# Kernel tuning notes

Hardware: AMD Instinct MI355X
Metric: run time of the kernel (lower is better)

Reference implementation:

```python
import jax, jax.numpy as jnp
import numpy as np

BRANCH = 16    # tree branching factor
HEIGHT = 4     # tree height (levels below virtual root 0)
D_MODEL = 1024 # feature dim of Xi / model output
IN_DIM = 1024  # raw input dim
BATCH = 4096


def _build_tree(b, h):
    # Balanced b-ary tree. Node ids are 1-based in BFS order; id 0 is the
    # virtual root (df.parent == 0 selects level-1 nodes in the original).
    level_sizes = [b ** l for l in range(1, h + 1)]
    starts = np.cumsum([1] + level_sizes)[:-1]  # first id of each level
    n_nodes = int(sum(level_sizes))
    children = np.zeros((n_nodes + 1, b), dtype=np.int32)  # 0 == no child
    children[0] = np.arange(1, b + 1)  # root's children (parent == 0)
    for l in range(1, h):
        ids = np.arange(starts[l - 1], starts[l - 1] + level_sizes[l - 1])
        pos = np.arange(level_sizes[l - 1])
        children[ids] = starts[l] + pos[:, None] * b + np.arange(b)[None, :]
    return n_nodes, children


def setup_inputs() -> dict:
    key = jax.random.key(0)
    k1, k2, k3 = jax.random.split(key, 3)
    n_nodes, children = _build_tree(BRANCH, HEIGHT)
    X = jax.random.normal(k1, (BATCH, IN_DIM), dtype=jnp.float32)
    W = jax.random.normal(k2, (IN_DIM, D_MODEL), dtype=jnp.float32) / np.sqrt(IN_DIM)
    # Xi: [d_model, n_nodes] class-embedding matrix (angle-based -> unit columns)
    Xi = jax.random.normal(k3, (D_MODEL, n_nodes), dtype=jnp.float32)
    Xi = Xi / jnp.linalg.norm(Xi, axis=0, keepdims=True)
    return {"X": X, "W": W, "Xi": Xi, "children": jnp.asarray(children)}


def reference(X, W, Xi, children):
    # f = model(X); here the stand-in model is a linear layer.
    f = X @ W                      # [B, d]
    XiT = Xi.T                     # [n_nodes, d]
    B = X.shape[0]
    neg_inf = jnp.finfo(f.dtype).min

    cur = jnp.zeros((B,), dtype=jnp.int32)          # start at virtual root 0
    cols = [jnp.zeros((B,), dtype=jnp.int32)]       # y_pred[:, 0] == 0
    for _ in range(HEIGHT):
        cand = children[cur]                         # [B, K] 1-based ids, 0 = pad
        emb = XiT[cand - 1]                          # [B, K, d] (pad rows masked below)
        g = jnp.einsum('bkd,bd->bk', emb, f)         # scores vs candidate children
        valid = cand > 0
        g = jnp.where(valid, g, neg_inf)
        idx = jnp.argmax(g, axis=-1)
        nxt = jnp.take_along_axis(cand, idx[:, None], axis=1)[:, 0]
        any_valid = jnp.any(valid, axis=-1)          # False once a leaf is reached
        nxt = jnp.where(any_valid, nxt, 0)           # original leaves y_pred at 0
        cols.append(nxt)
        cur = jnp.where(any_valid, nxt, cur)         # stop descending at leaves
    return jnp.stack(cols, axis=1)                   # [B, HEIGHT+1] int32
```

## Files before the change

### kernel.cpp

```cpp
#include <hip/hip_runtime.h>
#include <hip/hip_bf16.h>
#include <cstdint>
#include <cfloat>

#define BATCH   4096
#define IN_DIM  1024
#define D_MODEL 1024
#define BRANCH  16
#define HEIGHT  4
#define N_NODES 69904

#define BM 128
#define BN 64
#define BK 16

__global__ __launch_bounds__(128) void gemm_f32(const float* __restrict__ A,
                                                const float* __restrict__ B,
                                                float* __restrict__ C) {
    __shared__ float As[BK][BM + 4];
    __shared__ float Bs[BK][BN + 4];

    const int t  = threadIdx.x;
    const int tx = t & 7;
    const int ty = t >> 3;
    const int bm = blockIdx.x;
    const int bn = blockIdx.y;

    const int arow = t >> 2;
    const int ac4  = (t & 3) * 4;
    const float* Ab = A + (size_t)bm * BM * IN_DIM;
    const float* Bb = B + (size_t)bn * BN;

    float4 ar[4], br[2];

#define LOAD_TILE(k0)                                                          \
    {                                                                          \
        _Pragma("unroll")                                                      \
        for (int i = 0; i < 4; ++i)                                            \
            ar[i] = *(const float4*)(Ab + (size_t)(arow + 32 * i) * IN_DIM +   \
                                     (k0) + ac4);                              \
        _Pragma("unroll")                                                      \
        for (int i = 0; i < 2; ++i) {                                          \
            int idx = t + 128 * i;                                             \
            br[i] = *(const float4*)(Bb + (size_t)((k0) + (idx >> 4)) * D_MODEL\
                                     + (idx & 15) * 4);                        \
        }                                                                      \
    }

#define STORE_TILE()                                                           \
    {                                                                          \
        _Pragma("unroll")                                                      \
        for (int i = 0; i < 4; ++i) {                                          \
            As[ac4 + 0][arow + 32 * i] = ar[i].x;                              \
            As[ac4 + 1][arow + 32 * i] = ar[i].y;                              \
            As[ac4 + 2][arow + 32 * i] = ar[i].z;                              \
            As[ac4 + 3][arow + 32 * i] = ar[i].w;                              \
        }                                                                      \
        _Pragma("unroll")                                                      \
        for (int i = 0; i < 2; ++i) {                                          \
            int idx = t + 128 * i;                                             \
            *(float4*)&Bs[idx >> 4][(idx & 15) * 4] = br[i];                   \
        }                                                                      \
    }

    float acc[8][8] = {};

#define COMPUTE_TILE()                                                         \
    {                                                                          \
        _Pragma("unroll")                                                      \
        for (int k = 0; k < BK; ++k) {                                         \
            float4 a0 = *(const float4*)&As[k][ty * 8];                        \
            float4 a1 = *(const float4*)&As[k][ty * 8 + 4];                    \
            float4 b0 = *(const float4*)&Bs[k][tx * 8];                        \
            float4 b1 = *(const float4*)&Bs[k][tx * 8 + 4];                    \
            const float aa[8] = {a0.x, a0.y, a0.z, a0.w, a1.x, a1.y, a1.z, a1.w};\
            const float bb[8] = {b0.x, b0.y, b0.z, b0.w, b1.x, b1.y, b1.z, b1.w};\
            _Pragma("unroll")                                                  \
            for (int i = 0; i < 8; ++i)                                        \
                _Pragma("unroll")                                              \
                for (int j = 0; j < 8; ++j)                                    \
                    acc[i][j] = fmaf(aa[i], bb[j], acc[i][j]);                 \
        }                                                                      \
    }

    LOAD_TILE(0);
    STORE_TILE();
    __syncthreads();

    for (int k0 = BK; k0 < IN_DIM; k0 += BK) {
        LOAD_TILE(k0);
        COMPUTE_TILE();
        __syncthreads();
        STORE_TILE();
        __syncthreads();
    }
    COMPUTE_TILE();

    float* Cb = C + (size_t)(bm * BM + ty * 8) * D_MODEL + bn * BN + tx * 8;
#pragma unroll
    for (int i = 0; i < 8; ++i) {
        float4 v0 = {acc[i][0], acc[i][1], acc[i][2], acc[i][3]};
        float4 v1 = {acc[i][4], acc[i][5], acc[i][6], acc[i][7]};
        *(float4*)(Cb + (size_t)i * D_MODEL)     = v0;
        *(float4*)(Cb + (size_t)i * D_MODEL + 4) = v1;
    }
#undef LOAD_TILE
#undef STORE_TILE
#undef COMPUTE_TILE
}

__global__ __launch_bounds__(256) void descend(const float* __restrict__ f,
                                               const float* __restrict__ Xi,
                                               const int* __restrict__ children,
                                               int* __restrict__ out) {
    __shared__ float fs[4][1024];

    const int lane = threadIdx.x & 63;
    const int w    = threadIdx.x >> 6;
    const int b    = blockIdx.x * 4 + w;

    {
        const float4* frow = (const float4*)(f + (size_t)b * D_MODEL);
        float4* fsw = (float4*)fs[w];
#pragma unroll
        for (int i = 0; i < 4; ++i) fsw[lane + 64 * i] = frow[lane + 64 * i];
    }
    __syncthreads();

    const int q  = lane & 3;
    const int dg = lane >> 2;
    const float* frd = fs[w] + dg;

    int cur = 0;
    if (lane == 0) out[(size_t)b * (HEIGHT + 1)] = 0;

    for (int lev = 0; lev < HEIGHT; ++lev) {
        const int child0 = __builtin_amdgcn_readfirstlane(children[cur * BRANCH]);
        const float* xp = Xi + (size_t)dg * N_NODES + (child0 - 1) + q * 4;

        float4 acc = {0.f, 0.f, 0.f, 0.f};
#pragma unroll 8
        for (int t = 0; t < 64; ++t) {
            float4 x = *(const float4*)xp;
            float fv = frd[16 * t];
            acc.x = fmaf(fv, x.x, acc.x);
            acc.y = fmaf(fv, x.y, acc.y);
            acc.z = fmaf(fv, x.z, acc.z);
            acc.w = fmaf(fv, x.w, acc.w);
            xp += (size_t)16 * N_NODES;
        }

#pragma unroll
        for (int m = 4; m <= 32; m <<= 1) {
            acc.x += __shfl_xor(acc.x, m);
            acc.y += __shfl_xor(acc.y, m);
            acc.z += __shfl_xor(acc.z, m);
            acc.w += __shfl_xor(acc.w, m);
        }

        float bv = acc.x; int bc = q * 4;
        if (acc.y > bv) { bv = acc.y; bc = q * 4 + 1; }
        if (acc.z > bv) { bv = acc.z; bc = q * 4 + 2; }
        if (acc.w > bv) { bv = acc.w; bc = q * 4 + 3; }

#pragma unroll
        for (int m = 1; m <= 2; m <<= 1) {
            float ov = __shfl_xor(bv, m);
            int   oc = __shfl_xor(bc, m);
            if (ov > bv || (ov == bv && oc < bc)) { bv = ov; bc = oc; }
        }

        const int nxt = child0 + bc;
        if (lane == 0) out[(size_t)b * (HEIGHT + 1) + lev + 1] = nxt;
        cur = nxt;
    }
}

extern "C" void kernel_launch(void* const* d_in, const int* in_sizes, int n_in,
                              void* d_out, int out_size, void* d_ws, size_t ws_size,
                              hipStream_t stream) {
    const float* X        = (const float*)d_in[0];
    const float* W        = (const float*)d_in[1];
    const float* Xi       = (const float*)d_in[2];
    const int*   children = (const int*)d_in[3];
    int* out = (int*)d_out;

    float* f = (float*)d_ws;

    dim3 ggrid(BATCH / BM, D_MODEL / BN);
    gemm_f32<<<ggrid, 128, 0, stream>>>(X, W, f);

    descend<<<BATCH / 4, 256, 0, stream>>>(f, Xi, children, out);
}
```

Baseline: 617.8 us.

## Widen GEMM tile to 128x128 and split descent dot products across two waves

```diff
diff --git a/kernel.cpp b/kernel.cpp
--- a/kernel.cpp
+++ b/kernel.cpp
@@ -11,56 +11,55 @@
 #define N_NODES 69904
 
 #define BM 128
-#define BN 64
+#define BN 128
 #define BK 16
 
-__global__ __launch_bounds__(128) void gemm_f32(const float* __restrict__ A,
+__global__ __launch_bounds__(256) void gemm_f32(const float* __restrict__ A,
                                                 const float* __restrict__ B,
                                                 float* __restrict__ C) {
     __shared__ float As[BK][BM + 4];
     __shared__ float Bs[BK][BN + 4];
 
     const int t  = threadIdx.x;
-    const int tx = t & 7;
-    const int ty = t >> 3;
+    const int tx = t & 15;
+    const int ty = t >> 4;
     const int bm = blockIdx.x;
     const int bn = blockIdx.y;
 
     const int arow = t >> 2;
     const int ac4  = (t & 3) * 4;
+    const int brow = t >> 5;
+    const int bc4  = (t & 31) * 4;
+
     const float* Ab = A + (size_t)bm * BM * IN_DIM;
     const float* Bb = B + (size_t)bn * BN;
 
-    float4 ar[4], br[2];
+    float4 ar[2], br[2];
 
 #define LOAD_TILE(k0)                                                          \
     {                                                                          \
         _Pragma("unroll")                                                      \
-        for (int i = 0; i < 4; ++i)                                            \
-            ar[i] = *(const float4*)(Ab + (size_t)(arow + 32 * i) * IN_DIM +   \
+        for (int i = 0; i < 2; ++i)                                            \
+            ar[i] = *(const float4*)(Ab + (size_t)(arow + 64 * i) * IN_DIM +   \
                                      (k0) + ac4);                              \
         _Pragma("unroll")                                                      \
-        for (int i = 0; i < 2; ++i) {                                          \
-            int idx = t + 128 * i;                                             \
-            br[i] = *(const float4*)(Bb + (size_t)((k0) + (idx >> 4)) * D_MODEL\
-                                     + (idx & 15) * 4);                        \
-        }                                                                      \
+        for (int i = 0; i < 2; ++i)                                            \
+            br[i] = *(const float4*)(Bb + (size_t)((k0) + brow + 8 * i) *      \
+                                     D_MODEL + bc4);                           \
     }
 
 #define STORE_TILE()                                                           \
     {                                                                          \
         _Pragma("unroll")                                                      \
-        for (int i = 0; i < 4; ++i) {                                          \
-            As[ac4 + 0][arow + 32 * i] = ar[i].x;                              \
-            As[ac4 + 1][arow + 32 * i] = ar[i].y;                              \
-            As[ac4 + 2][arow + 32 * i] = ar[i].z;                              \
-            As[ac4 + 3][arow + 32 * i] = ar[i].w;                              \
+        for (int i = 0; i < 2; ++i) {                                          \
+            As[ac4 + 0][arow + 64 * i] = ar[i].x;                              \
+            As[ac4 + 1][arow + 64 * i] = ar[i].y;                              \
+            As[ac4 + 2][arow + 64 * i] = ar[i].z;                              \
+            As[ac4 + 3][arow + 64 * i] = ar[i].w;                              \
         }                                                                      \
         _Pragma("unroll")                                                      \
-        for (int i = 0; i < 2; ++i) {                                          \
-            int idx = t + 128 * i;                                             \
-            *(float4*)&Bs[idx >> 4][(idx & 15) * 4] = br[i];                   \
-        }                                                                      \
+        for (int i = 0; i < 2; ++i)                                            \
+            *(float4*)&Bs[brow + 8 * i][bc4] = br[i];                          \
     }
 
     float acc[8][8] = {};
@@ -71,8 +70,8 @@
         for (int k = 0; k < BK; ++k) {                                         \
             float4 a0 = *(const float4*)&As[k][ty * 8];                        \
             float4 a1 = *(const float4*)&As[k][ty * 8 + 4];                    \
-            float4 b0 = *(const float4*)&Bs[k][tx * 8];                        \
-            float4 b1 = *(const float4*)&Bs[k][tx * 8 + 4];                    \
+            float4 b0 = *(const float4*)&Bs[k][tx * 4];                        \
+            float4 b1 = *(const float4*)&Bs[k][tx * 4 + 64];                   \
             const float aa[8] = {a0.x, a0.y, a0.z, a0.w, a1.x, a1.y, a1.z, a1.w};\
             const float bb[8] = {b0.x, b0.y, b0.z, b0.w, b1.x, b1.y, b1.z, b1.w};\
             _Pragma("unroll")                                                  \
@@ -96,53 +95,61 @@
     }
     COMPUTE_TILE();
 
-    float* Cb = C + (size_t)(bm * BM + ty * 8) * D_MODEL + bn * BN + tx * 8;
+    float* Cb = C + (size_t)(bm * BM + ty * 8) * D_MODEL + bn * BN;
 #pragma unroll
     for (int i = 0; i < 8; ++i) {
         float4 v0 = {acc[i][0], acc[i][1], acc[i][2], acc[i][3]};
         float4 v1 = {acc[i][4], acc[i][5], acc[i][6], acc[i][7]};
-        *(float4*)(Cb + (size_t)i * D_MODEL)     = v0;
-        *(float4*)(Cb + (size_t)i * D_MODEL + 4) = v1;
+        *(float4*)(Cb + (size_t)i * D_MODEL + tx * 4)      = v0;
+        *(float4*)(Cb + (size_t)i * D_MODEL + tx * 4 + 64) = v1;
     }
 #undef LOAD_TILE
 #undef STORE_TILE
 #undef COMPUTE_TILE
 }
 
-__global__ __launch_bounds__(256) void descend(const float* __restrict__ f,
-                                               const float* __restrict__ Xi,
-                                               const int* __restrict__ children,
-                                               int* __restrict__ out) {
-    __shared__ float fs[4][1024];
-
-    const int lane = threadIdx.x & 63;
-    const int w    = threadIdx.x >> 6;
-    const int b    = blockIdx.x * 4 + w;
+__global__ __launch_bounds__(256, 6) void descend(const float* __restrict__ f,
+                                                  const float* __restrict__ Xi,
+                                                  const int* __restrict__ children,
+                                                  int* __restrict__ out) {
+    __shared__ float  fs[2][1024];
+    __shared__ float4 part[2][2][4];
+
+    const int t    = threadIdx.x;
+    const int lane = t & 63;
+    const int w    = t >> 6;
+    const int r    = w >> 1;
+    const int h    = w & 1;
+    const int b    = blockIdx.x * 2 + r;
 
     {
-        const float4* frow = (const float4*)(f + (size_t)b * D_MODEL);
-        float4* fsw = (float4*)fs[w];
-#pragma unroll
-        for (int i = 0; i < 4; ++i) fsw[lane + 64 * i] = frow[lane + 64 * i];
-    }
-    __syncthreads();
+        const float4* src = (const float4*)(f + (size_t)blockIdx.x * 2 * D_MODEL);
+        float4* dst = (float4*)fs;
+        dst[t]       = src[t];
+        dst[t + 256] = src[t + 256];
+    }
 
     const int q  = lane & 3;
     const int dg = lane >> 2;
-    const float* frd = fs[w] + dg;
+    const float*  frd   = fs[r] + h * 512 + dg;
+    const size_t  dbase = (size_t)(h * 512 + dg) * N_NODES;
+
+    if (w == 0 && lane == 0) out[(size_t)b * (HEIGHT + 1)] = 0;
+    if (w == 2 && lane == 0) out[(size_t)(b) * (HEIGHT + 1)] = 0;
+
+    __syncthreads();
 
     int cur = 0;
-    if (lane == 0) out[(size_t)b * (HEIGHT + 1)] = 0;
-
     for (int lev = 0; lev < HEIGHT; ++lev) {
-        const int child0 = __builtin_amdgcn_readfirstlane(children[cur * BRANCH]);
-        const float* xp = Xi + (size_t)dg * N_NODES + (child0 - 1) + q * 4;
+        const int child0 = __builtin_amdgcn_readfirstlane(
+            children[(size_t)cur * BRANCH]);
+        const float* xp = Xi + dbase + (size_t)(child0 - 1) + q * 4;
 
         float4 acc = {0.f, 0.f, 0.f, 0.f};
 #pragma unroll 8
-        for (int t = 0; t < 64; ++t) {
-            float4 x = *(const float4*)xp;
-            float fv = frd[16 * t];
+        for (int i = 0; i < 32; ++i) {
+            float4 x  = *(const float4*)xp;
+            float  fv = frd[16 * i];
             acc.x = fmaf(fv, x.x, acc.x);
             acc.y = fmaf(fv, x.y, acc.y);
             acc.z = fmaf(fv, x.z, acc.z);
@@ -157,12 +164,17 @@
             acc.z += __shfl_xor(acc.z, m);
             acc.w += __shfl_xor(acc.w, m);
         }
-
-        float bv = acc.x; int bc = q * 4;
-        if (acc.y > bv) { bv = acc.y; bc = q * 4 + 1; }
-        if (acc.z > bv) { bv = acc.z; bc = q * 4 + 2; }
-        if (acc.w > bv) { bv = acc.w; bc = q * 4 + 3; }
-
+        if (lane < 4) part[r][h][lane] = acc;
+        __syncthreads();
+
+        const float4 s0 = part[r][0][q];
+        const float4 s1 = part[r][1][q];
+        const float sv[4] = {s0.x + s1.x, s0.y + s1.y, s0.z + s1.z, s0.w + s1.w};
+        float bv = sv[0];
+        int   bc = q * 4;
+#pragma unroll
+        for (int j = 1; j < 4; ++j)
+            if (sv[j] > bv) { bv = sv[j]; bc = q * 4 + j; }
 #pragma unroll
         for (int m = 1; m <= 2; m <<= 1) {
             float ov = __shfl_xor(bv, m);
@@ -170,9 +182,10 @@
             if (ov > bv || (ov == bv && oc < bc)) { bv = ov; bc = oc; }
         }
 
-        const int nxt = child0 + bc;
-        if (lane == 0) out[(size_t)b * (HEIGHT + 1) + lev + 1] = nxt;
-        cur = nxt;
+        cur = child0 + bc;
+        if (h == 0 && lane == 0)
+            out[(size_t)b * (HEIGHT + 1) + lev + 1] = cur;
+        __syncthreads();
     }
 }
 
@@ -188,7 +201,7 @@
     float* f = (float*)d_ws;
 
     dim3 ggrid(BATCH / BM, D_MODEL / BN);
-    gemm_f32<<<ggrid, 128, 0, stream>>>(X, W, f);
-
-    descend<<<BATCH / 4, 256, 0, stream>>>(f, Xi, children, out);
+    gemm_f32<<<ggrid, 256, 0, stream>>>(X, W, f);
+
+    descend<<<BATCH / 2, 256, 0, stream>>>(f, Xi, children, out);
 }
```

After: 613.7 us. No clear change (-0.7%).

## Repack Xi into contiguous per-parent child tiles, fused with a wider GEMM

Applied to the files above, without the earlier changes.

```diff
diff --git a/kernel.cpp b/kernel.cpp
--- a/kernel.cpp
+++ b/kernel.cpp
@@ -1,7 +1,5 @@
 #include <hip/hip_runtime.h>
-#include <hip/hip_bf16.h>
 #include <cstdint>
-#include <cfloat>
 
 #define BATCH   4096
 #define IN_DIM  1024
@@ -9,121 +7,155 @@
 #define BRANCH  16
 #define HEIGHT  4
 #define N_NODES 69904
+#define N_TILES 4369
+#define TILE_ELEMS 16384
 
 #define BM 128
-#define BN 64
+#define BN 128
 #define BK 16
 
-__global__ __launch_bounds__(128) void gemm_f32(const float* __restrict__ A,
-                                                const float* __restrict__ B,
-                                                float* __restrict__ C) {
-    __shared__ float As[BK][BM + 4];
-    __shared__ float Bs[BK][BN + 4];
-
-    const int t  = threadIdx.x;
-    const int tx = t & 7;
-    const int ty = t >> 3;
-    const int bm = blockIdx.x;
-    const int bn = blockIdx.y;
-
-    const int arow = t >> 2;
-    const int ac4  = (t & 3) * 4;
-    const float* Ab = A + (size_t)bm * BM * IN_DIM;
-    const float* Bb = B + (size_t)bn * BN;
-
-    float4 ar[4], br[2];
+__global__ __launch_bounds__(256) void phase1(const float* __restrict__ X,
+                                              const float* __restrict__ W,
+                                              const float* __restrict__ Xi,
+                                              float* __restrict__ f,
+                                              float* __restrict__ XiP) {
+    __shared__ float4 smem4[2064];
+    const int bid = blockIdx.x;
+    const int t   = threadIdx.x;
+
+    if (bid < 256) {
+        float* As = (float*)smem4;
+        float* Bs = (float*)smem4 + BK * (BM + 4);
+#define AS(k, m) As[(k) * (BM + 4) + (m)]
+#define BS(k, n) Bs[(k) * (BN + 4) + (n)]
+        const int tx = t & 15, ty = t >> 4;
+        const int bm = bid >> 3, bn = bid & 7;
+        const int arow = t >> 2, ac4 = (t & 3) * 4;
+        const int brow = t >> 5, bc4 = (t & 31) * 4;
+        const float* Ab = X + (size_t)bm * BM * IN_DIM;
+        const float* Bb = W + (size_t)bn * BN;
+        float4 ar[2], br[2];
+        float acc[8][8] = {};
 
 #define LOAD_TILE(k0)                                                          \
-    {                                                                          \
-        _Pragma("unroll")                                                      \
-        for (int i = 0; i < 4; ++i)                                            \
-            ar[i] = *(const float4*)(Ab + (size_t)(arow + 32 * i) * IN_DIM +   \
-                                     (k0) + ac4);                              \
-        _Pragma("unroll")                                                      \
-        for (int i = 0; i < 2; ++i) {                                          \
-            int idx = t + 128 * i;                                             \
-            br[i] = *(const float4*)(Bb + (size_t)((k0) + (idx >> 4)) * D_MODEL\
-                                     + (idx & 15) * 4);                        \
-        }                                                                      \
-    }
-
+        {                                                                      \
+            _Pragma("unroll")                                                  \
+            for (int i = 0; i < 2; ++i)                                        \
+                ar[i] = *(const float4*)(Ab + (size_t)(arow + 64 * i) * IN_DIM \
+                                         + (k0) + ac4);                        \
+            _Pragma("unroll")                                                  \
+            for (int i = 0; i < 2; ++i)                                        \
+                br[i] = *(const float4*)(Bb + (size_t)((k0) + brow + 8 * i) *  \
+                                         D_MODEL + bc4);                       \
+        }
 #define STORE_TILE()                                                           \
-    {                                                                          \
-        _Pragma("unroll")                                                      \
-        for (int i = 0; i < 4; ++i) {                                          \
-            As[ac4 + 0][arow + 32 * i] = ar[i].x;                              \
-            As[ac4 + 1][arow + 32 * i] = ar[i].y;                              \
-            As[ac4 + 2][arow + 32 * i] = ar[i].z;                              \
-            As[ac4 + 3][arow + 32 * i] = ar[i].w;                              \
-        }                                                                      \
-        _Pragma("unroll")                                                      \
-        for (int i = 0; i < 2; ++i) {                                          \
-            int idx = t + 128 * i;                                             \
-            *(float4*)&Bs[idx >> 4][(idx & 15) * 4] = br[i];                   \
-        }                                                                      \
-    }
-
-    float acc[8][8] = {};
-
+        {                                                                      \
+            _Pragma("unroll")                                                  \
+            for (int i = 0; i < 2; ++i) {                                      \
+                AS(ac4 + 0, arow + 64 * i) = ar[i].x;                          \
+                AS(ac4 + 1, arow + 64 * i) = ar[i].y;                          \
+                AS(ac4 + 2, arow + 64 * i) = ar[i].z;                          \
+                AS(ac4 + 3, arow + 64 * i) = ar[i].w;                          \
+            }                                                                  \
+            _Pragma("unroll")                                                  \
+            for (int i = 0; i < 2; ++i)                                        \
+                *(float4*)&BS(brow + 8 * i, bc4) = br[i];                      \
+        }
 #define COMPUTE_TILE()                                                         \
-    {                                                                          \
-        _Pragma("unroll")                                                      \
-        for (int k = 0; k < BK; ++k) {                                         \
-            float4 a0 = *(const float4*)&As[k][ty * 8];                        \
-            float4 a1 = *(const float4*)&As[k][ty * 8 + 4];                    \
-            float4 b0 = *(const float4*)&Bs[k][tx * 8];                        \
-            float4 b1 = *(const float4*)&Bs[k][tx * 8 + 4];                    \
-            const float aa[8] = {a0.x, a0.y, a0.z, a0.w, a1.x, a1.y, a1.z, a1.w};\
-            const float bb[8] = {b0.x, b0.y, b0.z, b0.w, b1.x, b1.y, b1.z, b1.w};\
-            _Pragma("unroll")                                                  \
-            for (int i = 0; i < 8; ++i)                                        \
+        {                                                                      \
+            _Pragma("unroll")                                                  \
+            for (int k = 0; k < BK; ++k) {                                     \
+                float4 a0 = *(const float4*)&AS(k, ty * 8);                    \
+                float4 a1 = *(const float4*)&AS(k, ty * 8 + 4);                \
+                float4 b0 = *(const float4*)&BS(k, tx * 4);                    \
+                float4 b1 = *(const float4*)&BS(k, tx * 4 + 64);               \
+                const float aa[8] = {a0.x, a0.y, a0.z, a0.w,                   \
+                                     a1.x, a1.y, a1.z, a1.w};                  \
+                const float bb[8] = {b0.x, b0.y, b0.z, b0.w,                   \
+                                     b1.x, b1.y, b1.z, b1.w};                  \
                 _Pragma("unroll")                                              \
-                for (int j = 0; j < 8; ++j)                                    \
-                    acc[i][j] = fmaf(aa[i], bb[j], acc[i][j]);                 \
-        }                                                                      \
-    }
-
-    LOAD_TILE(0);
-    STORE_TILE();
-    __syncthreads();
-
-    for (int k0 = BK; k0 < IN_DIM; k0 += BK) {
-        LOAD_TILE(k0);
-        COMPUTE_TILE();
-        __syncthreads();
+                for (int i = 0; i < 8; ++i)                                    \
+                    _Pragma("unroll")                                          \
+                    for (int j = 0; j < 8; ++j)                                \
+                        acc[i][j] = fmaf(aa[i], bb[j], acc[i][j]);             \
+            }                                                                  \
+        }
+
+        LOAD_TILE(0);
         STORE_TILE();
         __syncthreads();
-    }
-    COMPUTE_TILE();
-
-    float* Cb = C + (size_t)(bm * BM + ty * 8) * D_MODEL + bn * BN + tx * 8;
-#pragma unroll
-    for (int i = 0; i < 8; ++i) {
-        float4 v0 = {acc[i][0], acc[i][1], acc[i][2], acc[i][3]};
-        float4 v1 = {acc[i][4], acc[i][5], acc[i][6], acc[i][7]};
-        *(float4*)(Cb + (size_t)i * D_MODEL)     = v0;
-        *(float4*)(Cb + (size_t)i * D_MODEL + 4) = v1;
-    }
+        for (int k0 = BK; k0 < IN_DIM; k0 += BK) {
+            LOAD_TILE(k0);
+            COMPUTE_TILE();
+            __syncthreads();
+            STORE_TILE();
+            __syncthreads();
+        }
+        COMPUTE_TILE();
+
+        float* Cb = f + (size_t)(bm * BM + ty * 8) * D_MODEL + bn * BN;
+#pragma unroll
+        for (int i = 0; i < 8; ++i) {
+            float4 v0 = {acc[i][0], acc[i][1], acc[i][2], acc[i][3]};
+            float4 v1 = {acc[i][4], acc[i][5], acc[i][6], acc[i][7]};
+            *(float4*)(Cb + (size_t)i * D_MODEL + tx * 4)      = v0;
+            *(float4*)(Cb + (size_t)i * D_MODEL + tx * 4 + 64) = v1;
+        }
 #undef LOAD_TILE
 #undef STORE_TILE
 #undef COMPUTE_TILE
+#undef AS
+#undef BS
+    } else {
+        float4 (*S)[129] = (float4(*)[129])smem4;
+        const int rid = bid - 256;
+        const int pg  = rid >> 6;
+        const int dc  = rid & 63;
+        const int c0  = pg << 9;
+        const int d0  = dc << 4;
+
+#pragma unroll
+        for (int j = 0; j < 8; ++j) {
+            const int idx = j * 256 + t;
+            const int dr  = idx >> 7;
+            const int c4  = idx & 127;
+            const int col = c0 + (c4 << 2);
+            if (col < N_NODES)
+                S[dr][c4] = *(const float4*)(Xi + (size_t)(d0 + dr) * N_NODES
+                                             + col);
+        }
+        __syncthreads();
+#pragma unroll
+        for (int j = 0; j < 8; ++j) {
+            const int idx = j * 256 + t;
+            const int pl  = idx >> 6;
+            const int dr  = (idx >> 2) & 15;
+            const int kq  = idx & 3;
+            const int p   = (pg << 5) + pl;
+            if (p < N_TILES) {
+                float4 v = S[dr][(pl << 2) + kq];
+                *(float4*)(XiP + (size_t)p * TILE_ELEMS +
+                           (size_t)(d0 + dr) * 16 + (kq << 2)) = v;
+            }
+        }
+    }
 }
 
 __global__ __launch_bounds__(256) void descend(const float* __restrict__ f,
-                                               const float* __restrict__ Xi,
-                                               const int* __restrict__ children,
+                                               const float* __restrict__ XiP,
                                                int* __restrict__ out) {
     __shared__ float fs[4][1024];
 
-    const int lane = threadIdx.x & 63;
-    const int w    = threadIdx.x >> 6;
+    const int t    = threadIdx.x;
+    const int lane = t & 63;
+    const int w    = t >> 6;
     const int b    = blockIdx.x * 4 + w;
 
     {
-        const float4* frow = (const float4*)(f + (size_t)b * D_MODEL);
-        float4* fsw = (float4*)fs[w];
-#pragma unroll
-        for (int i = 0; i < 4; ++i) fsw[lane + 64 * i] = frow[lane + 64 * i];
+        const float4* src = (const float4*)(f + (size_t)blockIdx.x * 4 * D_MODEL);
+        float4* dst = (float4*)fs;
+#pragma unroll
+        for (int i = 0; i < 4; ++i) dst[t + 256 * i] = src[t + 256 * i];
     }
     __syncthreads();
 
@@ -135,19 +167,17 @@
     if (lane == 0) out[(size_t)b * (HEIGHT + 1)] = 0;
 
     for (int lev = 0; lev < HEIGHT; ++lev) {
-        const int child0 = __builtin_amdgcn_readfirstlane(children[cur * BRANCH]);
-        const float* xp = Xi + (size_t)dg * N_NODES + (child0 - 1) + q * 4;
+        const float* tp = XiP + (size_t)cur * TILE_ELEMS + 4 * lane;
 
         float4 acc = {0.f, 0.f, 0.f, 0.f};
 #pragma unroll 8
-        for (int t = 0; t < 64; ++t) {
-            float4 x = *(const float4*)xp;
-            float fv = frd[16 * t];
+        for (int i = 0; i < 64; ++i) {
+            float4 x  = *(const float4*)(tp + 256 * i);
+            float  fv = frd[16 * i];
             acc.x = fmaf(fv, x.x, acc.x);
             acc.y = fmaf(fv, x.y, acc.y);
             acc.z = fmaf(fv, x.z, acc.z);
             acc.w = fmaf(fv, x.w, acc.w);
-            xp += (size_t)16 * N_NODES;
         }
 
 #pragma unroll
@@ -162,7 +192,6 @@
         if (acc.y > bv) { bv = acc.y; bc = q * 4 + 1; }
         if (acc.z > bv) { bv = acc.z; bc = q * 4 + 2; }
         if (acc.w > bv) { bv = acc.w; bc = q * 4 + 3; }
-
 #pragma unroll
         for (int m = 1; m <= 2; m <<= 1) {
             float ov = __shfl_xor(bv, m);
@@ -170,25 +199,24 @@
             if (ov > bv || (ov == bv && oc < bc)) { bv = ov; bc = oc; }
         }
 
-        const int nxt = child0 + bc;
-        if (lane == 0) out[(size_t)b * (HEIGHT + 1) + lev + 1] = nxt;
-        cur = nxt;
+        cur = 16 * cur + 1 + bc;
+        if (lane == 0) out[(size_t)b * (HEIGHT + 1) + lev + 1] = cur;
     }
 }
 
 extern "C" void kernel_launch(void* const* d_in, const int* in_sizes, int n_in,
                               void* d_out, int out_size, void* d_ws, size_t ws_size,
                               hipStream_t stream) {
-    const float* X        = (const float*)d_in[0];
-    const float* W        = (const float*)d_in[1];
-    const float* Xi       = (const float*)d_in[2];
-    const int*   children = (const int*)d_in[3];
+    const float* X  = (const float*)d_in[0];
+    const float* W  = (const float*)d_in[1];
+    const float* Xi = (const float*)d_in[2];
     int* out = (int*)d_out;
 
-    float* f = (float*)d_ws;
-
-    dim3 ggrid(BATCH / BM, D_MODEL / BN);
-    gemm_f32<<<ggrid, 128, 0, stream>>>(X, W, f);
-
-    descend<<<BATCH / 4, 256, 0, stream>>>(f, Xi, children, out);
+    float* f   = (float*)d_ws;
+    float* XiP = (float*)d_ws + (size_t)BATCH * D_MODEL;
+
+    const int repack_blocks = 137 * 64;
+    phase1<<<256 + repack_blocks, 256, 0, stream>>>(X, W, Xi, f, XiP);
+
+    descend<<<BATCH / 4, 256, 0, stream>>>(f, XiP, out);
 }
```

Result: slower. 652.3 us (+5.6%).
